# Kernel optimization log

Hardware: AMD Instinct MI355X
Metric: run time of the kernel (lower is better)

The kernel has to match this reference:

```python
import jax, jax.numpy as jnp
import numpy as np

N, E, IN, OUT, H = 20000, 640000, 256, 64, 4


def setup_inputs() -> dict:
    key = jax.random.key(0)
    ks = jax.random.split(key, 10)
    x = jax.random.normal(ks[0], (N, IN), dtype=jnp.float32)
    edge_index = jax.random.randint(ks[1], (2, E), 0, N, dtype=jnp.int64)
    s1 = 1.0 / np.sqrt(IN)
    s2 = 1.0 / np.sqrt(H * OUT)
    return {
        "x": x,
        "edge_index": edge_index,
        "W1": jax.random.normal(ks[2], (IN, H * OUT), dtype=jnp.float32) * s1,
        "att_src1": jax.random.normal(ks[3], (H, OUT), dtype=jnp.float32) * s2,
        "att_dst1": jax.random.normal(ks[4], (H, OUT), dtype=jnp.float32) * s2,
        "bias1": jnp.zeros((H * OUT,), dtype=jnp.float32),
        "W2": jax.random.normal(ks[5], (H * OUT, OUT), dtype=jnp.float32) * s2,
        "att_src2": jax.random.normal(ks[6], (1, OUT), dtype=jnp.float32) * (1.0 / np.sqrt(OUT)),
        "att_dst2": jax.random.normal(ks[7], (1, OUT), dtype=jnp.float32) * (1.0 / np.sqrt(OUT)),
        "bias2": jnp.zeros((OUT,), dtype=jnp.float32),
    }


def _gat_layer(x, src, dst, W, att_src, att_dst, bias, concat):
    n = x.shape[0]
    h_, c = att_src.shape
    h = (x @ W).reshape(n, h_, c)                     # [N,H,C]
    a_src = jnp.einsum("nhc,hc->nh", h, att_src)      # [N,H]
    a_dst = jnp.einsum("nhc,hc->nh", h, att_dst)
    e = jax.nn.leaky_relu(a_src[src] + a_dst[dst], 0.2)  # [E,H]
    m = jax.ops.segment_max(e, dst, num_segments=n)
    e = jnp.exp(e - m[dst])
    denom = jax.ops.segment_sum(e, dst, num_segments=n)
    alpha = e / (denom[dst] + 1e-16)                  # edge softmax over dst groups
    out = jax.ops.segment_sum(alpha[:, :, None] * h[src], dst, num_segments=n)  # [N,H,C]
    out = out.reshape(n, h_ * c) if concat else out.mean(axis=1)
    return out + bias


def reference(x, edge_index, W1, att_src1, att_dst1, bias1, W2, att_src2, att_dst2, bias2):
    n = x.shape[0]
    loops = jnp.arange(n, dtype=edge_index.dtype)
    ei = jnp.concatenate([edge_index, jnp.stack([loops, loops])], axis=1)  # add self-loops
    src, dst = ei[0], ei[1]
    # eval mode: dropout layers are identity
    x1 = jax.nn.elu(_gat_layer(x, src, dst, W1, att_src1, att_dst1, bias1, concat=True))
    x2 = _gat_layer(x1, src, dst, W2, att_src2, att_dst2, bias2, concat=False)
    return x2
```

## Files before the change

### kernel.cpp

```cpp
#include <hip/hip_runtime.h>
#include <math.h>

#define NN   20000
#define INF  256
#define HID  256
#define NH   4
#define OUTF 64

__device__ __forceinline__ float lrelu(float x){ return x > 0.f ? x : 0.2f*x; }
__device__ __forceinline__ float elu(float x){ return x > 0.f ? x : __expf(x)-1.f; }

__global__ void k_deg_init(int* deg){
    int i = blockIdx.x*blockDim.x + threadIdx.x;
    if (i < NN) deg[i] = 1;
}

__global__ void k_deg_hist(const int* __restrict__ ei, int* deg, int E){
    int e = blockIdx.x*blockDim.x + threadIdx.x;
    if (e < E) atomicAdd(&deg[ei[E + e]], 1);
}

__global__ void k_scan(const int* __restrict__ deg, int* __restrict__ rowptr){
    __shared__ int part[1024];
    int t = threadIdx.x;
    const int CH = 20;
    int base = t*CH;
    int s = 0;
    for (int i = 0; i < CH; i++){ int idx = base+i; if (idx < NN) s += deg[idx]; }
    part[t] = s;
    __syncthreads();
    for (int off = 1; off < 1024; off <<= 1){
        int v = (t >= off) ? part[t-off] : 0;
        __syncthreads();
        part[t] += v;
        __syncthreads();
    }
    int run = (t > 0) ? part[t-1] : 0;
    for (int i = 0; i < CH; i++){
        int idx = base+i;
        if (idx < NN){ rowptr[idx] = run; run += deg[idx]; }
    }
    if (t == 1023) rowptr[NN] = part[1023];
}

__global__ void k_selfloop(const int* __restrict__ rowptr, int* col, int* cursor){
    int n = blockIdx.x*blockDim.x + threadIdx.x;
    if (n < NN){ int p = rowptr[n]; col[p] = n; cursor[n] = p+1; }
}

__global__ void k_scatter(const int* __restrict__ ei, int* cursor, int* col, int E){
    int e = blockIdx.x*blockDim.x + threadIdx.x;
    if (e < E){
        int s = ei[e], d = ei[E + e];
        int pos = atomicAdd(&cursor[d], 1);
        col[pos] = s;
    }
}

__global__ void k_gemm1(const float* __restrict__ x, const float* __restrict__ W,
                        const float* __restrict__ att_s, const float* __restrict__ att_d,
                        float* __restrict__ h1, float* __restrict__ as1,
                        float* __restrict__ ad1){
    __shared__ float xs[16][INF];
    int row0 = blockIdx.x*16;
    int t = threadIdx.x;
    int lane = t & 63, wv = t >> 6;
    for (int i = t; i < 16*INF; i += 256)
        xs[i>>8][i&255] = x[(size_t)(row0 + (i>>8))*INF + (i&255)];
    __syncthreads();
    float acc[16];
    #pragma unroll
    for (int r = 0; r < 16; r++) acc[r] = 0.f;
    for (int k = 0; k < INF; k++){
        float w = W[k*HID + t];
        #pragma unroll
        for (int r = 0; r < 16; r++) acc[r] = fmaf(xs[r][k], w, acc[r]);
    }
    float sv = att_s[t], dv = att_d[t];
    #pragma unroll
    for (int r = 0; r < 16; r++){
        h1[(size_t)(row0+r)*HID + t] = acc[r];
        float ps = acc[r]*sv, pd = acc[r]*dv;
        #pragma unroll
        for (int off = 32; off >= 1; off >>= 1){
            ps += __shfl_xor(ps, off, 64);
            pd += __shfl_xor(pd, off, 64);
        }
        if (lane == 0){
            as1[(row0+r)*NH + wv] = ps;
            ad1[(row0+r)*NH + wv] = pd;
        }
    }
}

__global__ void k_agg1(const float* __restrict__ h1, const int* __restrict__ rowptr,
                       const int* __restrict__ col, const float* __restrict__ as1,
                       const float* __restrict__ ad1, const float* __restrict__ bias,
                       float* __restrict__ x1){
    int wv = threadIdx.x >> 6, lane = threadIdx.x & 63;
    int n = blockIdx.x*4 + wv;
    if (n >= NN) return;
    int beg = rowptr[n], end = rowptr[n+1];
    float4 adst = ((const float4*)ad1)[n];
    int h = lane >> 4;
    float adh = h==0?adst.x : h==1?adst.y : h==2?adst.z : adst.w;
    float den = 0.f;
    float4 acc0 = {0,0,0,0}, acc1 = {0,0,0,0};

    for (int base = beg; base < end; base += 64){
        int cnt = min(64, end - base);
        int myidx = (lane < cnt) ? col[base + lane] : 0;
        int j = 0;
        for (; j + 4 <= cnt; j += 4){
            int s0 = __shfl(myidx, j,   64);
            int s1 = __shfl(myidx, j+1, 64);
            int s2 = __shfl(myidx, j+2, 64);
            int s3 = __shfl(myidx, j+3, 64);
            float4 hv0 = ((const float4*)(h1 + (size_t)s0*HID))[lane];
            float4 hv1 = ((const float4*)(h1 + (size_t)s1*HID))[lane];
            float4 hv2 = ((const float4*)(h1 + (size_t)s2*HID))[lane];
            float4 hv3 = ((const float4*)(h1 + (size_t)s3*HID))[lane];
            float4 a0 = ((const float4*)as1)[s0];
            float4 a1 = ((const float4*)as1)[s1];
            float4 a2 = ((const float4*)as1)[s2];
            float4 a3 = ((const float4*)as1)[s3];
            float e0 = h==0?a0.x : h==1?a0.y : h==2?a0.z : a0.w;
            float e1 = h==0?a1.x : h==1?a1.y : h==2?a1.z : a1.w;
            float e2 = h==0?a2.x : h==1?a2.y : h==2?a2.z : a2.w;
            float e3 = h==0?a3.x : h==1?a3.y : h==2?a3.z : a3.w;
            float w0 = __expf(lrelu(e0+adh));
            float w1 = __expf(lrelu(e1+adh));
            float w2 = __expf(lrelu(e2+adh));
            float w3 = __expf(lrelu(e3+adh));
            den += (w0 + w1) + (w2 + w3);
            acc0.x = fmaf(w0, hv0.x, acc0.x); acc0.y = fmaf(w0, hv0.y, acc0.y);
            acc0.z = fmaf(w0, hv0.z, acc0.z); acc0.w = fmaf(w0, hv0.w, acc0.w);
            acc1.x = fmaf(w1, hv1.x, acc1.x); acc1.y = fmaf(w1, hv1.y, acc1.y);
            acc1.z = fmaf(w1, hv1.z, acc1.z); acc1.w = fmaf(w1, hv1.w, acc1.w);
            acc0.x = fmaf(w2, hv2.x, acc0.x); acc0.y = fmaf(w2, hv2.y, acc0.y);
            acc0.z = fmaf(w2, hv2.z, acc0.z); acc0.w = fmaf(w2, hv2.w, acc0.w);
            acc1.x = fmaf(w3, hv3.x, acc1.x); acc1.y = fmaf(w3, hv3.y, acc1.y);
            acc1.z = fmaf(w3, hv3.z, acc1.z); acc1.w = fmaf(w3, hv3.w, acc1.w);
        }
        for (; j < cnt; j++){
            int s0 = __shfl(myidx, j, 64);
            float4 hv0 = ((const float4*)(h1 + (size_t)s0*HID))[lane];
            float4 a0 = ((const float4*)as1)[s0];
            float e0 = h==0?a0.x : h==1?a0.y : h==2?a0.z : a0.w;
            float w0 = __expf(lrelu(e0+adh));
            den += w0;
            acc0.x = fmaf(w0, hv0.x, acc0.x); acc0.y = fmaf(w0, hv0.y, acc0.y);
            acc0.z = fmaf(w0, hv0.z, acc0.z); acc0.w = fmaf(w0, hv0.w, acc0.w);
        }
    }
    float rs = 1.f/(den + 1e-16f);
    float4 b = ((const float4*)bias)[lane];
    float4 o;
    o.x = elu((acc0.x+acc1.x)*rs + b.x);
    o.y = elu((acc0.y+acc1.y)*rs + b.y);
    o.z = elu((acc0.z+acc1.z)*rs + b.z);
    o.w = elu((acc0.w+acc1.w)*rs + b.w);
    ((float4*)(x1 + (size_t)n*HID))[lane] = o;
}

__global__ void k_gemm2(const float* __restrict__ x1, const float* __restrict__ W2,
                        const float* __restrict__ att_s, const float* __restrict__ att_d,
                        float* __restrict__ h2, float* __restrict__ a2s,
                        float* __restrict__ a2d){
    __shared__ float xs[32][HID];
    int row0 = blockIdx.x*32;
    int t = threadIdx.x;
    for (int i = t; i < 32*HID; i += 256)
        xs[i>>8][i&255] = x1[(size_t)(row0 + (i>>8))*HID + (i&255)];
    __syncthreads();
    int c  = t & 63;
    int r0 = (t >> 6)*8;
    float acc[8];
    #pragma unroll
    for (int r = 0; r < 8; r++) acc[r] = 0.f;
    for (int k = 0; k < HID; k++){
        float w = W2[k*OUTF + c];
        #pragma unroll
        for (int r = 0; r < 8; r++) acc[r] = fmaf(xs[r0+r][k], w, acc[r]);
    }
    float sv = att_s[c], dv = att_d[c];
    #pragma unroll
    for (int r = 0; r < 8; r++){
        h2[(size_t)(row0+r0+r)*OUTF + c] = acc[r];
        float ps = acc[r]*sv, pd = acc[r]*dv;
        #pragma unroll
        for (int off = 32; off >= 1; off >>= 1){
            ps += __shfl_xor(ps, off, 64);
            pd += __shfl_xor(pd, off, 64);
        }
        if (c == 0){
            a2s[row0+r0+r] = ps;
            a2d[row0+r0+r] = pd;
        }
    }
}

__global__ void k_agg2(const float* __restrict__ h2, const int* __restrict__ rowptr,
                       const int* __restrict__ col, const float* __restrict__ a2s,
                       const float* __restrict__ a2d, const float* __restrict__ bias2,
                       float* __restrict__ out){
    int wv = threadIdx.x >> 6, lane = threadIdx.x & 63;
    int n = blockIdx.x*4 + wv;
    if (n >= NN) return;
    int beg = rowptr[n], end = rowptr[n+1];
    float adh = a2d[n];
    float den = 0.f;
    float acc0 = 0.f, acc1 = 0.f;
    for (int base = beg; base < end; base += 64){
        int cnt = min(64, end - base);
        int myidx = (lane < cnt) ? col[base + lane] : 0;
        int j = 0;
        for (; j + 4 <= cnt; j += 4){
            int s0 = __shfl(myidx, j,   64);
            int s1 = __shfl(myidx, j+1, 64);
            int s2 = __shfl(myidx, j+2, 64);
            int s3 = __shfl(myidx, j+3, 64);
            float hv0 = h2[(size_t)s0*OUTF + lane];
            float hv1 = h2[(size_t)s1*OUTF + lane];
            float hv2 = h2[(size_t)s2*OUTF + lane];
            float hv3 = h2[(size_t)s3*OUTF + lane];
            float w0 = __expf(lrelu(a2s[s0]+adh));
            float w1 = __expf(lrelu(a2s[s1]+adh));
            float w2 = __expf(lrelu(a2s[s2]+adh));
            float w3 = __expf(lrelu(a2s[s3]+adh));
            den += (w0+w1)+(w2+w3);
            acc0 = fmaf(w0, hv0, acc0);
            acc1 = fmaf(w1, hv1, acc1);
            acc0 = fmaf(w2, hv2, acc0);
            acc1 = fmaf(w3, hv3, acc1);
        }
        for (; j < cnt; j++){
            int s0 = __shfl(myidx, j, 64);
            float hv0 = h2[(size_t)s0*OUTF + lane];
            float w0 = __expf(lrelu(a2s[s0]+adh));
            den += w0;
            acc0 = fmaf(w0, hv0, acc0);
        }
    }
    out[(size_t)n*OUTF + lane] = (acc0+acc1)/(den + 1e-16f) + bias2[lane];
}

extern "C" void kernel_launch(void* const* d_in, const int* in_sizes, int n_in,
                              void* d_out, int out_size, void* d_ws, size_t ws_size,
                              hipStream_t stream){
    const float* x      = (const float*)d_in[0];
    const int*   ei     = (const int*)  d_in[1];
    const float* W1     = (const float*)d_in[2];
    const float* att_s1 = (const float*)d_in[3];
    const float* att_d1 = (const float*)d_in[4];
    const float* bias1  = (const float*)d_in[5];
    const float* W2     = (const float*)d_in[6];
    const float* att_s2 = (const float*)d_in[7];
    const float* att_d2 = (const float*)d_in[8];
    const float* bias2  = (const float*)d_in[9];
    int E = in_sizes[1] / 2;

    char* w = (char*)d_ws;
    size_t off = 0;
    auto alloc = [&](size_t b){ void* p = w + off; off += (b + 255) & ~(size_t)255; return p; };
    float* h1     = (float*)alloc((size_t)NN*HID*4);
    float* x1     = (float*)alloc((size_t)NN*HID*4);
    float* h2     = (float*)alloc((size_t)NN*OUTF*4);
    float* as1    = (float*)alloc((size_t)NN*NH*4);
    float* ad1    = (float*)alloc((size_t)NN*NH*4);
    float* a2s    = (float*)alloc((size_t)NN*4);
    float* a2d    = (float*)alloc((size_t)NN*4);
    int*   deg    = (int*)alloc((size_t)(NN+1)*4);
    int*   rowptr = (int*)alloc((size_t)(NN+1)*4);
    int*   cursor = (int*)alloc((size_t)NN*4);
    int*   col    = (int*)alloc((size_t)(E+NN)*4);

    k_deg_init<<<(NN+255)/256, 256, 0, stream>>>(deg);
    k_deg_hist<<<(E+255)/256, 256, 0, stream>>>(ei, deg, E);
    k_scan<<<1, 1024, 0, stream>>>(deg, rowptr);
    k_selfloop<<<(NN+255)/256, 256, 0, stream>>>(rowptr, col, cursor);
    k_scatter<<<(E+255)/256, 256, 0, stream>>>(ei, cursor, col, E);

    k_gemm1<<<NN/16, 256, 0, stream>>>(x, W1, att_s1, att_d1, h1, as1, ad1);
    k_agg1<<<(NN+3)/4, 256, 0, stream>>>(h1, rowptr, col, as1, ad1, bias1, x1);

    k_gemm2<<<NN/32, 256, 0, stream>>>(x1, W2, att_s2, att_d2, h2, a2s, a2d);
    k_agg2<<<(NN+3)/4, 256, 0, stream>>>(h2, rowptr, col, a2s, a2d, bias2, (float*)d_out);
}
```

Baseline: 377.9 us.

## Store layer-1 features in bf16 and unroll gather loops by eight

Measured after the change: 324.8 us. 14.1% less time.

```diff
diff --git a/kernel.cpp b/kernel.cpp
--- a/kernel.cpp
+++ b/kernel.cpp
@@ -1,4 +1,5 @@
 #include <hip/hip_runtime.h>
+#include <hip/hip_bf16.h>
 #include <math.h>
 
 #define NN   20000
@@ -59,7 +60,7 @@
 
 __global__ void k_gemm1(const float* __restrict__ x, const float* __restrict__ W,
                         const float* __restrict__ att_s, const float* __restrict__ att_d,
-                        float* __restrict__ h1, float* __restrict__ as1,
+                        __hip_bfloat16* __restrict__ h1b, float* __restrict__ as1,
                         float* __restrict__ ad1){
     __shared__ float xs[16][INF];
     int row0 = blockIdx.x*16;
@@ -79,7 +80,7 @@
     float sv = att_s[t], dv = att_d[t];
     #pragma unroll
     for (int r = 0; r < 16; r++){
-        h1[(size_t)(row0+r)*HID + t] = acc[r];
+        h1b[(size_t)(row0+r)*HID + t] = __float2bfloat16(acc[r]);
         float ps = acc[r]*sv, pd = acc[r]*dv;
         #pragma unroll
         for (int off = 32; off >= 1; off >>= 1){
@@ -93,7 +94,7 @@
     }
 }
 
-__global__ void k_agg1(const float* __restrict__ h1, const int* __restrict__ rowptr,
+__global__ void k_agg1(const ushort* __restrict__ h1b, const int* __restrict__ rowptr,
                        const int* __restrict__ col, const float* __restrict__ as1,
                        const float* __restrict__ ad1, const float* __restrict__ bias,
                        float* __restrict__ x1){
@@ -105,61 +106,58 @@
     int h = lane >> 4;
     float adh = h==0?adst.x : h==1?adst.y : h==2?adst.z : adst.w;
     float den = 0.f;
-    float4 acc0 = {0,0,0,0}, acc1 = {0,0,0,0};
+    float4 accs[4];
+    #pragma unroll
+    for (int u = 0; u < 4; u++) accs[u] = make_float4(0.f,0.f,0.f,0.f);
 
     for (int base = beg; base < end; base += 64){
         int cnt = min(64, end - base);
         int myidx = (lane < cnt) ? col[base + lane] : 0;
         int j = 0;
-        for (; j + 4 <= cnt; j += 4){
-            int s0 = __shfl(myidx, j,   64);
-            int s1 = __shfl(myidx, j+1, 64);
-            int s2 = __shfl(myidx, j+2, 64);
-            int s3 = __shfl(myidx, j+3, 64);
-            float4 hv0 = ((const float4*)(h1 + (size_t)s0*HID))[lane];
-            float4 hv1 = ((const float4*)(h1 + (size_t)s1*HID))[lane];
-            float4 hv2 = ((const float4*)(h1 + (size_t)s2*HID))[lane];
-            float4 hv3 = ((const float4*)(h1 + (size_t)s3*HID))[lane];
-            float4 a0 = ((const float4*)as1)[s0];
-            float4 a1 = ((const float4*)as1)[s1];
-            float4 a2 = ((const float4*)as1)[s2];
-            float4 a3 = ((const float4*)as1)[s3];
-            float e0 = h==0?a0.x : h==1?a0.y : h==2?a0.z : a0.w;
-            float e1 = h==0?a1.x : h==1?a1.y : h==2?a1.z : a1.w;
-            float e2 = h==0?a2.x : h==1?a2.y : h==2?a2.z : a2.w;
-            float e3 = h==0?a3.x : h==1?a3.y : h==2?a3.z : a3.w;
-            float w0 = __expf(lrelu(e0+adh));
-            float w1 = __expf(lrelu(e1+adh));
-            float w2 = __expf(lrelu(e2+adh));
-            float w3 = __expf(lrelu(e3+adh));
-            den += (w0 + w1) + (w2 + w3);
-            acc0.x = fmaf(w0, hv0.x, acc0.x); acc0.y = fmaf(w0, hv0.y, acc0.y);
-            acc0.z = fmaf(w0, hv0.z, acc0.z); acc0.w = fmaf(w0, hv0.w, acc0.w);
-            acc1.x = fmaf(w1, hv1.x, acc1.x); acc1.y = fmaf(w1, hv1.y, acc1.y);
-            acc1.z = fmaf(w1, hv1.z, acc1.z); acc1.w = fmaf(w1, hv1.w, acc1.w);
-            acc0.x = fmaf(w2, hv2.x, acc0.x); acc0.y = fmaf(w2, hv2.y, acc0.y);
-            acc0.z = fmaf(w2, hv2.z, acc0.z); acc0.w = fmaf(w2, hv2.w, acc0.w);
-            acc1.x = fmaf(w3, hv3.x, acc1.x); acc1.y = fmaf(w3, hv3.y, acc1.y);
-            acc1.z = fmaf(w3, hv3.z, acc1.z); acc1.w = fmaf(w3, hv3.w, acc1.w);
+        for (; j + 8 <= cnt; j += 8){
+            int ss[8];
+            #pragma unroll
+            for (int u = 0; u < 8; u++) ss[u] = __shfl(myidx, j+u, 64);
+            uint2 hv[8];
+            float aw[8];
+            #pragma unroll
+            for (int u = 0; u < 8; u++){
+                hv[u] = *(const uint2*)(h1b + ((size_t)ss[u]<<8) + (lane<<2));
+                aw[u] = as1[ss[u]*NH + h];
+            }
+            #pragma unroll
+            for (int u = 0; u < 8; u++){
+                float w = __expf(lrelu(aw[u]+adh));
+                den += w;
+                float f0 = __uint_as_float(hv[u].x << 16);
+                float f1 = __uint_as_float(hv[u].x & 0xFFFF0000u);
+                float f2 = __uint_as_float(hv[u].y << 16);
+                float f3 = __uint_as_float(hv[u].y & 0xFFFF0000u);
+                accs[u&3].x = fmaf(w, f0, accs[u&3].x);
+                accs[u&3].y = fmaf(w, f1, accs[u&3].y);
+                accs[u&3].z = fmaf(w, f2, accs[u&3].z);
+                accs[u&3].w = fmaf(w, f3, accs[u&3].w);
+            }
         }
         for (; j < cnt; j++){
             int s0 = __shfl(myidx, j, 64);
-            float4 hv0 = ((const float4*)(h1 + (size_t)s0*HID))[lane];
-            float4 a0 = ((const float4*)as1)[s0];
-            float e0 = h==0?a0.x : h==1?a0.y : h==2?a0.z : a0.w;
-            float w0 = __expf(lrelu(e0+adh));
-            den += w0;
-            acc0.x = fmaf(w0, hv0.x, acc0.x); acc0.y = fmaf(w0, hv0.y, acc0.y);
-            acc0.z = fmaf(w0, hv0.z, acc0.z); acc0.w = fmaf(w0, hv0.w, acc0.w);
+            uint2 hv0 = *(const uint2*)(h1b + ((size_t)s0<<8) + (lane<<2));
+            float aw0 = as1[s0*NH + h];
+            float w = __expf(lrelu(aw0+adh));
+            den += w;
+            accs[0].x = fmaf(w, __uint_as_float(hv0.x << 16),        accs[0].x);
+            accs[0].y = fmaf(w, __uint_as_float(hv0.x & 0xFFFF0000u), accs[0].y);
+            accs[0].z = fmaf(w, __uint_as_float(hv0.y << 16),        accs[0].z);
+            accs[0].w = fmaf(w, __uint_as_float(hv0.y & 0xFFFF0000u), accs[0].w);
         }
     }
     float rs = 1.f/(den + 1e-16f);
     float4 b = ((const float4*)bias)[lane];
     float4 o;
-    o.x = elu((acc0.x+acc1.x)*rs + b.x);
-    o.y = elu((acc0.y+acc1.y)*rs + b.y);
-    o.z = elu((acc0.z+acc1.z)*rs + b.z);
-    o.w = elu((acc0.w+acc1.w)*rs + b.w);
+    o.x = elu((accs[0].x+accs[1].x+accs[2].x+accs[3].x)*rs + b.x);
+    o.y = elu((accs[0].y+accs[1].y+accs[2].y+accs[3].y)*rs + b.y);
+    o.z = elu((accs[0].z+accs[1].z+accs[2].z+accs[3].z)*rs + b.z);
+    o.w = elu((accs[0].w+accs[1].w+accs[2].w+accs[3].w)*rs + b.w);
     ((float4*)(x1 + (size_t)n*HID))[lane] = o;
 }
 
@@ -210,39 +208,37 @@
     int beg = rowptr[n], end = rowptr[n+1];
     float adh = a2d[n];
     float den = 0.f;
-    float acc0 = 0.f, acc1 = 0.f;
+    float acc[4] = {0.f, 0.f, 0.f, 0.f};
     for (int base = beg; base < end; base += 64){
         int cnt = min(64, end - base);
         int myidx = (lane < cnt) ? col[base + lane] : 0;
         int j = 0;
-        for (; j + 4 <= cnt; j += 4){
-            int s0 = __shfl(myidx, j,   64);
-            int s1 = __shfl(myidx, j+1, 64);
-            int s2 = __shfl(myidx, j+2, 64);
-            int s3 = __shfl(myidx, j+3, 64);
-            float hv0 = h2[(size_t)s0*OUTF + lane];
-            float hv1 = h2[(size_t)s1*OUTF + lane];
-            float hv2 = h2[(size_t)s2*OUTF + lane];
-            float hv3 = h2[(size_t)s3*OUTF + lane];
-            float w0 = __expf(lrelu(a2s[s0]+adh));
-            float w1 = __expf(lrelu(a2s[s1]+adh));
-            float w2 = __expf(lrelu(a2s[s2]+adh));
-            float w3 = __expf(lrelu(a2s[s3]+adh));
-            den += (w0+w1)+(w2+w3);
-            acc0 = fmaf(w0, hv0, acc0);
-            acc1 = fmaf(w1, hv1, acc1);
-            acc0 = fmaf(w2, hv2, acc0);
-            acc1 = fmaf(w3, hv3, acc1);
+        for (; j + 8 <= cnt; j += 8){
+            int ss[8];
+            #pragma unroll
+            for (int u = 0; u < 8; u++) ss[u] = __shfl(myidx, j+u, 64);
+            float hw[8], aw[8];
+            #pragma unroll
+            for (int u = 0; u < 8; u++){
+                hw[u] = h2[(size_t)ss[u]*OUTF + lane];
+                aw[u] = a2s[ss[u]];
+            }
+            #pragma unroll
+            for (int u = 0; u < 8; u++){
+                float w = __expf(lrelu(aw[u]+adh));
+                den += w;
+                acc[u&3] = fmaf(w, hw[u], acc[u&3]);
+            }
         }
         for (; j < cnt; j++){
             int s0 = __shfl(myidx, j, 64);
             float hv0 = h2[(size_t)s0*OUTF + lane];
             float w0 = __expf(lrelu(a2s[s0]+adh));
             den += w0;
-            acc0 = fmaf(w0, hv0, acc0);
-        }
-    }
-    out[(size_t)n*OUTF + lane] = (acc0+acc1)/(den + 1e-16f) + bias2[lane];
+            acc[0] = fmaf(w0, hv0, acc[0]);
+        }
+    }
+    out[(size_t)n*OUTF + lane] = (acc[0]+acc[1]+acc[2]+acc[3])/(den + 1e-16f) + bias2[lane];
 }
 
 extern "C" void kernel_launch(void* const* d_in, const int* in_sizes, int n_in,
@@ -263,7 +259,7 @@
     char* w = (char*)d_ws;
     size_t off = 0;
     auto alloc = [&](size_t b){ void* p = w + off; off += (b + 255) & ~(size_t)255; return p; };
-    float* h1     = (float*)alloc((size_t)NN*HID*4);
+    __hip_bfloat16* h1b = (__hip_bfloat16*)alloc((size_t)NN*HID*2);
     float* x1     = (float*)alloc((size_t)NN*HID*4);
     float* h2     = (float*)alloc((size_t)NN*OUTF*4);
     float* as1    = (float*)alloc((size_t)NN*NH*4);
@@ -281,8 +277,8 @@
     k_selfloop<<<(NN+255)/256, 256, 0, stream>>>(rowptr, col, cursor);
     k_scatter<<<(E+255)/256, 256, 0, stream>>>(ei, cursor, col, E);
 
-    k_gemm1<<<NN/16, 256, 0, stream>>>(x, W1, att_s1, att_d1, h1, as1, ad1);
-    k_agg1<<<(NN+3)/4, 256, 0, stream>>>(h1, rowptr, col, as1, ad1, bias1, x1);
+    k_gemm1<<<NN/16, 256, 0, stream>>>(x, W1, att_s1, att_d1, h1b, as1, ad1);
+    k_agg1<<<(NN+3)/4, 256, 0, stream>>>((const ushort*)h1b, rowptr, col, as1, ad1, bias1, x1);
 
     k_gemm2<<<NN/32, 256, 0, stream>>>(x1, W2, att_s2, att_d2, h2, a2s, a2d);
     k_agg2<<<(NN+3)/4, 256, 0, stream>>>(h2, rowptr, col, a2s, a2d, bias2, (float*)d_out);
```
